# Optimization experiments

Measured on AMD Instinct MI355X. Metric: run time of the kernel, lower is better.

Reference implementation:

```python
import jax, jax.numpy as jnp
import numpy as np

N = 16384       # num_nodes
IN = 128        # in_features
OUT = 128       # out_features
E = 524288      # num edges
NG = 8          # FastKAN num_grids
GRID_MIN, GRID_MAX = -2.0, 2.0
LN_EPS = 1e-5


def setup_inputs() -> dict:
    key = jax.random.key(0)
    ks = jax.random.split(key, 6)
    x = jax.random.normal(ks[0], (N, IN), dtype=jnp.float32)
    edge_index = jax.random.randint(ks[1], (2, E), 0, N, dtype=jnp.int32)
    # FastKANLayer params
    ln_gamma = jnp.ones((IN,), jnp.float32)
    ln_beta = jnp.zeros((IN,), jnp.float32)
    # SplineLinear: trunc-normal-ish init with scale 0.1 (fast-kan default)
    spline_w = (jax.random.normal(ks[2], (OUT, IN * NG), jnp.float32)
                * (0.1 / np.sqrt(IN * NG)))
    base_w = jax.random.normal(ks[3], (OUT, IN), jnp.float32) / np.sqrt(IN)
    base_b = jnp.zeros((OUT,), jnp.float32)
    # GCNConv.bias
    bias = jax.random.normal(ks[4], (OUT,), jnp.float32) * 0.01
    return dict(x=x, edge_index=edge_index, ln_gamma=ln_gamma, ln_beta=ln_beta,
                spline_w=spline_w, base_w=base_w, base_b=base_b, bias=bias)


def _fastkan(x, ln_gamma, ln_beta, spline_w, base_w, base_b):
    # LayerNorm
    mu = jnp.mean(x, axis=-1, keepdims=True)
    var = jnp.mean((x - mu) ** 2, axis=-1, keepdims=True)
    h = (x - mu) * jax.lax.rsqrt(var + LN_EPS) * ln_gamma + ln_beta
    # Gaussian RBF basis over fixed grid
    grid = jnp.linspace(GRID_MIN, GRID_MAX, NG)
    denom = (GRID_MAX - GRID_MIN) / (NG - 1)
    basis = jnp.exp(-(((h[..., None] - grid) / denom) ** 2))  # [N, IN, NG]
    out = basis.reshape(x.shape[0], IN * NG) @ spline_w.T      # [N, OUT]
    out = out + jax.nn.silu(x) @ base_w.T + base_b             # base update
    return out


def reference(x, edge_index, ln_gamma, ln_beta, spline_w, base_w, base_b, bias):
    num_nodes = x.shape[0]
    # Dense symmetric adjacency, exactly as the torch module builds it
    adj = jnp.zeros((num_nodes, num_nodes), x.dtype)
    adj = adj.at[edge_index[0], edge_index[1]].set(1.0)
    adj = adj.at[edge_index[1], edge_index[0]].set(1.0)
    deg = jnp.sum(adj, axis=1)
    dis = 1.0 / jnp.sqrt(deg)
    norm_adj = adj * dis[:, None] * dis[None, :]
    support = _fastkan(x, ln_gamma, ln_beta, spline_w, base_w, base_b)
    return norm_adj @ support + bias
```

## Files before the change

kernel.cpp:

```cpp
#include <hip/hip_runtime.h>

#define N_NODES 16384
#define NE 524288
#define KDIM 1152
#define KPAD 1160
#define KSTEPS 36
#define NBUCK 1024
#define SBLK 512
#define SPB 2048
#define MROW 516
#define DCAP 256

typedef unsigned int uint32;
typedef unsigned short ushort;
typedef __attribute__((ext_vector_type(8))) short bf16x8;
typedef __attribute__((ext_vector_type(4))) float f32x4;

__device__ __forceinline__ ushort f2bf(float f) {
    unsigned u = __float_as_uint(f);
    unsigned r = (u + 0x7fffu + ((u >> 16) & 1u)) >> 16;
    return (ushort)r;
}
__device__ __forceinline__ float bflo(uint32 u) {
    return __uint_as_float(u << 16);
}
__device__ __forceinline__ float bfhi(uint32 u) {
    return __uint_as_float(u & 0xffff0000u);
}

__global__ __launch_bounds__(256) void pre_kernel(
    const int* __restrict__ ei, uint32* __restrict__ ebuf,
    uint32* __restrict__ ocnt, const float* __restrict__ sw,
    const float* __restrict__ bw, ushort* __restrict__ Wp) {
    const int t = threadIdx.x;
    if (blockIdx.x >= SBLK) {
        int idx = (blockIdx.x - SBLK) * 256 + t;
        int i  = idx & 7;
        int l  = (idx >> 3) & 63;
        int ct = (idx >> 9) & 7;
        int kk = idx >> 12;
        int k   = kk * 32 + ((l >> 4) << 3) + i;
        int col = ct * 16 + (l & 15);
        float v = (k < 1024) ? sw[col * 1024 + k] : bw[col * 128 + (k - 1024)];
        Wp[idx] = f2bf(v);
        return;
    }
    __shared__ int hcnt[NBUCK];
    __shared__ int lbase[NBUCK];
    __shared__ int ps[256];
    __shared__ uint32 st[SPB];
    for (int q = t; q < NBUCK; q += 256) hcnt[q] = 0;
    __syncthreads();

    int bk[8], sl[8];
    uint32 pk[8];
#pragma unroll
    for (int k = 0; k < 4; ++k) {
        int e = blockIdx.x * 1024 + k * 256 + t;
        int a = ei[e];
        int b = ei[NE + e];
        bk[2 * k]     = a >> 4;
        pk[2 * k]     = ((uint32)(a & 15) << 14) | (uint32)b;
        bk[2 * k + 1] = b >> 4;
        pk[2 * k + 1] = ((uint32)(b & 15) << 14) | (uint32)a;
        sl[2 * k]     = atomicAdd(&hcnt[bk[2 * k]], 1);
        sl[2 * k + 1] = atomicAdd(&hcnt[bk[2 * k + 1]], 1);
    }
    __syncthreads();

    int c[4], loc[4];
    int s = 0;
#pragma unroll
    for (int q = 0; q < 4; ++q) {
        c[q] = hcnt[t * 4 + q];
        loc[q] = s;
        s += c[q];
    }
    ps[t] = s;
    __syncthreads();
    for (int off = 1; off < 256; off <<= 1) {
        int v = ps[t];
        int add = (t >= off) ? ps[t - off] : 0;
        __syncthreads();
        ps[t] = v + add;
        __syncthreads();
    }
    const int base = (t == 0) ? 0 : ps[t - 1];
    uint32* oc = ocnt + (size_t)blockIdx.x * NBUCK;
#pragma unroll
    for (int q = 0; q < 4; ++q) {
        int e0 = base + loc[q];
        lbase[t * 4 + q] = e0;
        oc[t * 4 + q] = (uint32)e0 | ((uint32)c[q] << 16);
    }
    __syncthreads();

#pragma unroll
    for (int k = 0; k < 8; ++k) st[lbase[bk[k]] + sl[k]] = pk[k];
    __syncthreads();
    uint32* gout = ebuf + (size_t)blockIdx.x * SPB;
#pragma unroll
    for (int k = 0; k < 8; ++k) gout[t + k * 256] = st[t + k * 256];
}

__global__ __launch_bounds__(256) void mid_kernel(
    const uint32* __restrict__ ebuf, const uint32* __restrict__ ocnt,
    float* __restrict__ dis, int* __restrict__ degarr,
    ushort* __restrict__ dadj, const float* __restrict__ x,
    const float* __restrict__ gamma, const float* __restrict__ beta,
    const ushort* __restrict__ Wp, const float* __restrict__ base_b,
    ushort* __restrict__ S) {
    __shared__ __align__(16) ushort smem[16 * KPAD];
    const int t = threadIdx.x;
    const int lane = t & 63;
    const int w = t >> 6;

    if (blockIdx.x & 1) {
        uint32* mask = (uint32*)smem;
        const int bkt = blockIdx.x >> 1;
        for (int i = t; i < 16 * MROW; i += 256) mask[i] = 0;
        __syncthreads();

        for (int b = t; b < SBLK; b += 256) {
            uint32 oc = ocnt[(size_t)b * NBUCK + bkt];
            int off = (int)(oc & 0xFFFFu);
            int cn  = (int)(oc >> 16);
            const uint32* p = ebuf + (size_t)b * SPB + off;
            for (int s = 0; s < cn; ++s) {
                uint32 e = p[s];
                atomicOr(&mask[(e >> 14) * MROW + ((e & 16383) >> 5)],
                         1u << (e & 31));
            }
        }
        __syncthreads();

        for (int n = w * 4; n < w * 4 + 4; ++n) {
            const uint32* row = &mask[n * MROW];
            uint32 wd[8];
            int c = 0;
#pragma unroll
            for (int j = 0; j < 8; ++j) {
                wd[j] = row[lane + 64 * j];
                c += __popc(wd[j]);
            }
            int inc = c;
#pragma unroll
            for (int o = 1; o < 64; o <<= 1) {
                int v = __shfl_up(inc, o);
                if (lane >= o) inc += v;
            }
            int total = __shfl(inc, 63);
            int pos = inc - c;
            const int node = bkt * 16 + n;
            if (lane == 0) {
                dis[node] = rsqrtf((float)total);
                degarr[node] = total > DCAP ? DCAP : total;
            }
            ushort* drow = dadj + (size_t)node * DCAP;
#pragma unroll
            for (int j = 0; j < 8; ++j) {
                uint32 bits = wd[j];
                int base = (lane + 64 * j) * 32;
                while (bits) {
                    int b = __ffs(bits) - 1;
                    bits &= bits - 1;
                    if (pos < DCAP) drow[pos] = (ushort)(base + b);
                    ++pos;
                }
            }
        }
        return;
    }

    ushort* Bs = smem;
    const int nodeBase = (blockIdx.x >> 1) * 16;

    const float g0 = gamma[lane], g1 = gamma[lane + 64];
    const float be0 = beta[lane], be1 = beta[lane + 64];

    for (int n = w * 4; n < w * 4 + 4; ++n) {
        const int row = nodeBase + n;
        float f0 = x[(size_t)row * 128 + lane];
        float f1 = x[(size_t)row * 128 + lane + 64];
        float s = f0 + f1;
#pragma unroll
        for (int o = 32; o; o >>= 1) s += __shfl_xor(s, o);
        float mu = s * 0.0078125f;
        float d0 = f0 - mu, d1 = f1 - mu;
        float v = d0 * d0 + d1 * d1;
#pragma unroll
        for (int o = 32; o; o >>= 1) v += __shfl_xor(v, o);
        float rstd = rsqrtf(v * 0.0078125f + 1e-5f);
        float h0 = d0 * rstd * g0 + be0;
        float h1 = d1 * rstd * g1 + be1;
        ushort pk0[8] __attribute__((aligned(16)));
        ushort pk1[8] __attribute__((aligned(16)));
#pragma unroll
        for (int g = 0; g < 8; ++g) {
            float gv = -2.0f + (float)g * (4.0f / 7.0f);
            float z0 = (h0 - gv) * 1.75f;
            float z1 = (h1 - gv) * 1.75f;
            pk0[g] = f2bf(__expf(-z0 * z0));
            pk1[g] = f2bf(__expf(-z1 * z1));
        }
        *reinterpret_cast<uint4*>(&Bs[n * KPAD + lane * 8]) =
            *reinterpret_cast<const uint4*>(pk0);
        *reinterpret_cast<uint4*>(&Bs[n * KPAD + (lane + 64) * 8]) =
            *reinterpret_cast<const uint4*>(pk1);
        Bs[n * KPAD + 1024 + lane]      = f2bf(f0 / (1.0f + __expf(-f0)));
        Bs[n * KPAD + 1024 + lane + 64] = f2bf(f1 / (1.0f + __expf(-f1)));
    }
    __syncthreads();

    const int ct0 = w * 2;
    f32x4 acc0 = {0.f, 0.f, 0.f, 0.f};
    f32x4 acc1 = {0.f, 0.f, 0.f, 0.f};
    const ushort* ArowBase = &Bs[(lane & 15) * KPAD + (lane >> 4) * 8];
    const bf16x8* Wv = (const bf16x8*)Wp;
#pragma unroll 4
    for (int kk = 0; kk < KSTEPS; ++kk) {
        bf16x8 a = *reinterpret_cast<const bf16x8*>(ArowBase + kk * 32);
        bf16x8 b0 = Wv[(size_t)(kk * 8 + ct0) * 64 + lane];
        bf16x8 b1 = Wv[(size_t)(kk * 8 + ct0 + 1) * 64 + lane];
        acc0 = __builtin_amdgcn_mfma_f32_16x16x32_bf16(a, b0, acc0, 0, 0, 0);
        acc1 = __builtin_amdgcn_mfma_f32_16x16x32_bf16(a, b1, acc1, 0, 0, 0);
    }

    const int col0 = ct0 * 16 + (lane & 15);
    const int rbase = (lane >> 4) * 4;
    const float bb0 = base_b[col0];
    const float bb1 = base_b[col0 + 16];
#pragma unroll
    for (int r = 0; r < 4; ++r) {
        const int row = nodeBase + rbase + r;
        S[(size_t)row * 128 + col0]      = f2bf(acc0[r] + bb0);
        S[(size_t)row * 128 + col0 + 16] = f2bf(acc1[r] + bb1);
    }
}

__global__ __launch_bounds__(256) void aggregate_kernel(
    const int* __restrict__ degarr, const ushort* __restrict__ dadj,
    const ushort* __restrict__ S, const float* __restrict__ dis,
    const float* __restrict__ bias, float* __restrict__ out) {
    __shared__ ushort lst[2][DCAP];
    __shared__ float part[2][2][128];
    const int t = threadIdx.x;
    const int g = t >> 7;
    const int tl = t & 127;
    const int i = blockIdx.x * 2 + g;

    const int total = degarr[i];
    const ushort* drow = dadj + (size_t)i * DCAP;
    if (tl < total) lst[g][tl] = drow[tl];
    if (tl + 128 < total) lst[g][tl + 128] = drow[tl + 128];
    __syncthreads();

    const int lane = t & 63;
    const int wv = (t >> 6) & 1;
    const uint32* S32 = (const uint32*)S;
    float a0 = 0.f, a1 = 0.f;
    int idx = wv;
    for (; idx + 6 < total; idx += 8) {
        int j0 = lst[g][idx], j1 = lst[g][idx + 2];
        int j2 = lst[g][idx + 4], j3 = lst[g][idx + 6];
        float d0 = dis[j0], d1 = dis[j1], d2 = dis[j2], d3 = dis[j3];
        uint32 u0 = S32[(size_t)j0 * 64 + lane];
        uint32 u1 = S32[(size_t)j1 * 64 + lane];
        uint32 u2 = S32[(size_t)j2 * 64 + lane];
        uint32 u3 = S32[(size_t)j3 * 64 + lane];
        a0 += (d0 * bflo(u0) + d1 * bflo(u1)) + (d2 * bflo(u2) + d3 * bflo(u3));
        a1 += (d0 * bfhi(u0) + d1 * bfhi(u1)) + (d2 * bfhi(u2) + d3 * bfhi(u3));
    }
    for (; idx < total; idx += 2) {
        int j = lst[g][idx];
        float d = dis[j];
        uint32 u = S32[(size_t)j * 64 + lane];
        a0 += d * bflo(u);
        a1 += d * bfhi(u);
    }
    part[g][wv][lane * 2]     = a0;
    part[g][wv][lane * 2 + 1] = a1;
    __syncthreads();

    float v = part[g][0][tl] + part[g][1][tl];
    out[(size_t)i * 128 + tl] = v * dis[i] + bias[tl];
}

extern "C" void kernel_launch(void* const* d_in, const int* in_sizes, int n_in,
                              void* d_out, int out_size, void* d_ws, size_t ws_size,
                              hipStream_t stream) {
    const float* x        = (const float*)d_in[0];
    const int*   ei       = (const int*)d_in[1];
    const float* ln_gamma = (const float*)d_in[2];
    const float* ln_beta  = (const float*)d_in[3];
    const float* spline_w = (const float*)d_in[4];
    const float* base_w   = (const float*)d_in[5];
    const float* base_b   = (const float*)d_in[6];
    const float* bias     = (const float*)d_in[7];
    float* out = (float*)d_out;

    char* ws = (char*)d_ws;
    const size_t WP_OFF   = 0;
    const size_t DIS_OFF  = 294912;
    const size_t DEG_OFF  = 360448;
    const size_t DADJ_OFF = 425984;
    const size_t OCNT_OFF = 8814592;
    const size_t EBUF_OFF = 10911744;
    const size_t S_OFF    = 15106048;
    const size_t NEEDED   = 19300352;
    if (ws_size < NEEDED) return;

    ushort* Wp     = (ushort*)(ws + WP_OFF);
    float*  dis    = (float*)(ws + DIS_OFF);
    int*    degarr = (int*)(ws + DEG_OFF);
    ushort* dadj   = (ushort*)(ws + DADJ_OFF);
    uint32* ocnt   = (uint32*)(ws + OCNT_OFF);
    uint32* ebuf   = (uint32*)(ws + EBUF_OFF);
    ushort* S      = (ushort*)(ws + S_OFF);

    pre_kernel<<<SBLK + 576, 256, 0, stream>>>(ei, ebuf, ocnt,
                                               spline_w, base_w, Wp);
    mid_kernel<<<2048, 256, 0, stream>>>(ebuf, ocnt, dis, degarr, dadj,
                                         x, ln_gamma, ln_beta, Wp, base_b, S);
    aggregate_kernel<<<N_NODES / 2, 256, 0, stream>>>(degarr, dadj, S, dis,
                                                      bias, out);
}
```

Baseline: 68.80 us.

## Use fewer, larger edge-bucketing blocks and split mid-kernel bucket scan across threads

Cuts the edge-sorting blocks from 512 to 128, so each block buckets 4096 edges into an 8192-entry shared staging array. Slot assignment now uses a second pass that re-reads the edges and does atomics on the prefix bases, instead of keeping slots in registers. In the mid kernel, each of the 128 source blocks is scanned by two threads with interleaved strides, which shortens the per-bucket serial loop and removes the loop over blocks. The trade-off is reading edge_index twice, using more shared memory per block, and running fewer pre blocks (less parallelism), in exchange for fewer ocnt entries and less serial work in mid_kernel.

```diff
diff --git a/kernel.cpp b/kernel.cpp
--- a/kernel.cpp
+++ b/kernel.cpp
@@ -6,8 +6,8 @@
 #define KPAD 1160
 #define KSTEPS 36
 #define NBUCK 1024
-#define SBLK 512
-#define SPB 2048
+#define SBLK 128
+#define SPB 8192
 #define MROW 516
 #define DCAP 256
 
@@ -46,25 +46,19 @@
         return;
     }
     __shared__ int hcnt[NBUCK];
-    __shared__ int lbase[NBUCK];
     __shared__ int ps[256];
     __shared__ uint32 st[SPB];
     for (int q = t; q < NBUCK; q += 256) hcnt[q] = 0;
     __syncthreads();
 
-    int bk[8], sl[8];
-    uint32 pk[8];
-#pragma unroll
-    for (int k = 0; k < 4; ++k) {
-        int e = blockIdx.x * 1024 + k * 256 + t;
+    const int ebase = blockIdx.x * (NE / SBLK);
+#pragma unroll 4
+    for (int k = 0; k < 16; ++k) {
+        int e = ebase + k * 256 + t;
         int a = ei[e];
         int b = ei[NE + e];
-        bk[2 * k]     = a >> 4;
-        pk[2 * k]     = ((uint32)(a & 15) << 14) | (uint32)b;
-        bk[2 * k + 1] = b >> 4;
-        pk[2 * k + 1] = ((uint32)(b & 15) << 14) | (uint32)a;
-        sl[2 * k]     = atomicAdd(&hcnt[bk[2 * k]], 1);
-        sl[2 * k + 1] = atomicAdd(&hcnt[bk[2 * k + 1]], 1);
+        atomicAdd(&hcnt[a >> 4], 1);
+        atomicAdd(&hcnt[b >> 4], 1);
     }
     __syncthreads();
 
@@ -90,17 +84,26 @@
 #pragma unroll
     for (int q = 0; q < 4; ++q) {
         int e0 = base + loc[q];
-        lbase[t * 4 + q] = e0;
+        hcnt[t * 4 + q] = e0;
         oc[t * 4 + q] = (uint32)e0 | ((uint32)c[q] << 16);
     }
     __syncthreads();
 
-#pragma unroll
-    for (int k = 0; k < 8; ++k) st[lbase[bk[k]] + sl[k]] = pk[k];
-    __syncthreads();
+#pragma unroll 4
+    for (int k = 0; k < 16; ++k) {
+        int e = ebase + k * 256 + t;
+        int a = ei[e];
+        int b = ei[NE + e];
+        int sl = atomicAdd(&hcnt[a >> 4], 1);
+        st[sl] = ((uint32)(a & 15) << 14) | (uint32)b;
+        sl = atomicAdd(&hcnt[b >> 4], 1);
+        st[sl] = ((uint32)(b & 15) << 14) | (uint32)a;
+    }
+    __syncthreads();
+
     uint32* gout = ebuf + (size_t)blockIdx.x * SPB;
 #pragma unroll
-    for (int k = 0; k < 8; ++k) gout[t + k * 256] = st[t + k * 256];
+    for (int k = 0; k < SPB / 256; ++k) gout[t + k * 256] = st[t + k * 256];
 }
 
 __global__ __launch_bounds__(256) void mid_kernel(
@@ -121,12 +124,13 @@
         for (int i = t; i < 16 * MROW; i += 256) mask[i] = 0;
         __syncthreads();
 
-        for (int b = t; b < SBLK; b += 256) {
-            uint32 oc = ocnt[(size_t)b * NBUCK + bkt];
-            int off = (int)(oc & 0xFFFFu);
-            int cn  = (int)(oc >> 16);
+        {
+            const int b = t & 127;
+            const uint32 oc = ocnt[(size_t)b * NBUCK + bkt];
+            const int off = (int)(oc & 0xFFFFu);
+            const int cn  = (int)(oc >> 16);
             const uint32* p = ebuf + (size_t)b * SPB + off;
-            for (int s = 0; s < cn; ++s) {
+            for (int s = (t >> 7); s < cn; s += 2) {
                 uint32 e = p[s];
                 atomicOr(&mask[(e >> 14) * MROW + ((e & 16383) >> 5)],
                          1u << (e & 31));
@@ -305,9 +309,9 @@
     const size_t DEG_OFF  = 360448;
     const size_t DADJ_OFF = 425984;
     const size_t OCNT_OFF = 8814592;
-    const size_t EBUF_OFF = 10911744;
-    const size_t S_OFF    = 15106048;
-    const size_t NEEDED   = 19300352;
+    const size_t EBUF_OFF = 9338880;
+    const size_t S_OFF    = 13533184;
+    const size_t NEEDED   = 17727488;
     if (ws_size < NEEDED) return;
 
     ushort* Wp     = (ushort*)(ws + WP_OFF);
```

After: 74.47 us. 8.2% more time.

## Double GEMM rows per block with split-K LDS phases and 2:1 role mix

Applied to the files above, without the earlier changes.

The GEMM half of mid_kernel now handles 32 nodes per block instead of 16, so each weight fragment loaded from global memory feeds two MFMAs. To keep LDS usage bounded, K is split into two phases of 576, and the weight packing is permuted so each phase covers 64 input channels' RBF and SiLU terms. Block roles change to two adjacency-bucket blocks per GEMM block, which keeps the grid at 1536 blocks. The ocnt loads are also hoisted ahead of the scan loop. The cost is more registers (8 cached rows per wave, 4 accumulators) and an extra barrier between phases.

```diff
diff --git a/kernel.cpp b/kernel.cpp
--- a/kernel.cpp
+++ b/kernel.cpp
@@ -3,8 +3,9 @@
 #define N_NODES 16384
 #define NE 524288
 #define KDIM 1152
-#define KPAD 1160
-#define KSTEPS 36
+#define KPH 576
+#define KPAD2 584
+#define KSTEPS_PH 18
 #define NBUCK 1024
 #define SBLK 512
 #define SPB 2048
@@ -39,9 +40,19 @@
         int l  = (idx >> 3) & 63;
         int ct = (idx >> 9) & 7;
         int kk = idx >> 12;
-        int k   = kk * 32 + ((l >> 4) << 3) + i;
+        int kp  = kk * 32 + ((l >> 4) << 3) + i;
+        int p   = kp / KPH;
+        int r   = kp - p * KPH;
         int col = ct * 16 + (l & 15);
-        float v = (k < 1024) ? sw[col * 1024 + k] : bw[col * 128 + (k - 1024)];
+        float v;
+        if (r < 512) {
+            int ch = p * 64 + (r >> 3);
+            int g  = r & 7;
+            v = sw[col * 1024 + ch * 8 + g];
+        } else {
+            int ch = p * 64 + (r - 512);
+            v = bw[col * 128 + ch];
+        }
         Wp[idx] = f2bf(v);
         return;
     }
@@ -110,19 +121,24 @@
     const float* __restrict__ gamma, const float* __restrict__ beta,
     const ushort* __restrict__ Wp, const float* __restrict__ base_b,
     ushort* __restrict__ S) {
-    __shared__ __align__(16) ushort smem[16 * KPAD];
+    __shared__ __align__(16) ushort smem[32 * KPAD2];
     const int t = threadIdx.x;
     const int lane = t & 63;
     const int w = t >> 6;
-
-    if (blockIdx.x & 1) {
+    const int role = blockIdx.x % 3;
+
+    if (role < 2) {
         uint32* mask = (uint32*)smem;
-        const int bkt = blockIdx.x >> 1;
+        const int bkt = (blockIdx.x / 3) * 2 + role;
         for (int i = t; i < 16 * MROW; i += 256) mask[i] = 0;
         __syncthreads();
 
-        for (int b = t; b < SBLK; b += 256) {
-            uint32 oc = ocnt[(size_t)b * NBUCK + bkt];
+        const uint32 oc0 = ocnt[(size_t)t * NBUCK + bkt];
+        const uint32 oc1 = ocnt[(size_t)(t + 256) * NBUCK + bkt];
+#pragma unroll
+        for (int h = 0; h < 2; ++h) {
+            const int b = h ? (t + 256) : t;
+            const uint32 oc = h ? oc1 : oc0;
             int off = (int)(oc & 0xFFFFu);
             int cn  = (int)(oc >> 16);
             const uint32* p = ebuf + (size_t)b * SPB + off;
@@ -173,13 +189,15 @@
     }
 
     ushort* Bs = smem;
-    const int nodeBase = (blockIdx.x >> 1) * 16;
+    const int nodeBase = (blockIdx.x / 3) * 32;
 
     const float g0 = gamma[lane], g1 = gamma[lane + 64];
     const float be0 = beta[lane], be1 = beta[lane + 64];
 
-    for (int n = w * 4; n < w * 4 + 4; ++n) {
-        const int row = nodeBase + n;
+    float h0r[8], h1r[8], f0r[8], f1r[8];
+#pragma unroll
+    for (int j = 0; j < 8; ++j) {
+        const int row = nodeBase + w * 8 + j;
         float f0 = x[(size_t)row * 128 + lane];
         float f1 = x[(size_t)row * 128 + lane + 64];
         float s = f0 + f1;
@@ -191,39 +209,54 @@
 #pragma unroll
         for (int o = 32; o; o >>= 1) v += __shfl_xor(v, o);
         float rstd = rsqrtf(v * 0.0078125f + 1e-5f);
-        float h0 = d0 * rstd * g0 + be0;
-        float h1 = d1 * rstd * g1 + be1;
-        ushort pk0[8] __attribute__((aligned(16)));
-        ushort pk1[8] __attribute__((aligned(16)));
-#pragma unroll
-        for (int g = 0; g < 8; ++g) {
-            float gv = -2.0f + (float)g * (4.0f / 7.0f);
-            float z0 = (h0 - gv) * 1.75f;
-            float z1 = (h1 - gv) * 1.75f;
-            pk0[g] = f2bf(__expf(-z0 * z0));
-            pk1[g] = f2bf(__expf(-z1 * z1));
-        }
-        *reinterpret_cast<uint4*>(&Bs[n * KPAD + lane * 8]) =
-            *reinterpret_cast<const uint4*>(pk0);
-        *reinterpret_cast<uint4*>(&Bs[n * KPAD + (lane + 64) * 8]) =
-            *reinterpret_cast<const uint4*>(pk1);
-        Bs[n * KPAD + 1024 + lane]      = f2bf(f0 / (1.0f + __expf(-f0)));
-        Bs[n * KPAD + 1024 + lane + 64] = f2bf(f1 / (1.0f + __expf(-f1)));
-    }
-    __syncthreads();
+        h0r[j] = d0 * rstd * g0 + be0;
+        h1r[j] = d1 * rstd * g1 + be1;
+        f0r[j] = f0;
+        f1r[j] = f1;
+    }
 
     const int ct0 = w * 2;
-    f32x4 acc0 = {0.f, 0.f, 0.f, 0.f};
-    f32x4 acc1 = {0.f, 0.f, 0.f, 0.f};
-    const ushort* ArowBase = &Bs[(lane & 15) * KPAD + (lane >> 4) * 8];
+    f32x4 accA = {0.f, 0.f, 0.f, 0.f};
+    f32x4 accB = {0.f, 0.f, 0.f, 0.f};
+    f32x4 accC = {0.f, 0.f, 0.f, 0.f};
+    f32x4 accD = {0.f, 0.f, 0.f, 0.f};
+    const ushort* Alo = &Bs[(lane & 15) * KPAD2 + (lane >> 4) * 8];
+    const ushort* Ahi = Alo + 16 * KPAD2;
     const bf16x8* Wv = (const bf16x8*)Wp;
-#pragma unroll 4
-    for (int kk = 0; kk < KSTEPS; ++kk) {
-        bf16x8 a = *reinterpret_cast<const bf16x8*>(ArowBase + kk * 32);
-        bf16x8 b0 = Wv[(size_t)(kk * 8 + ct0) * 64 + lane];
-        bf16x8 b1 = Wv[(size_t)(kk * 8 + ct0 + 1) * 64 + lane];
-        acc0 = __builtin_amdgcn_mfma_f32_16x16x32_bf16(a, b0, acc0, 0, 0, 0);
-        acc1 = __builtin_amdgcn_mfma_f32_16x16x32_bf16(a, b1, acc1, 0, 0, 0);
+
+#pragma unroll
+    for (int p = 0; p < 2; ++p) {
+        if (p) __syncthreads();
+#pragma unroll
+        for (int j = 0; j < 8; ++j) {
+            const int n = w * 8 + j;
+            const float h = p ? h1r[j] : h0r[j];
+            const float f = p ? f1r[j] : f0r[j];
+            ushort pk[8] __attribute__((aligned(16)));
+#pragma unroll
+            for (int g = 0; g < 8; ++g) {
+                float gv = -2.0f + (float)g * (4.0f / 7.0f);
+                float z = (h - gv) * 1.75f;
+                pk[g] = f2bf(__expf(-z * z));
+            }
+            *reinterpret_cast<uint4*>(&Bs[n * KPAD2 + lane * 8]) =
+                *reinterpret_cast<const uint4*>(pk);
+            Bs[n * KPAD2 + 512 + lane] = f2bf(f / (1.0f + __expf(-f)));
+        }
+        __syncthreads();
+
+#pragma unroll 3
+        for (int kkl = 0; kkl < KSTEPS_PH; ++kkl) {
+            const int kkg = p * KSTEPS_PH + kkl;
+            bf16x8 alo = *reinterpret_cast<const bf16x8*>(Alo + kkl * 32);
+            bf16x8 ahi = *reinterpret_cast<const bf16x8*>(Ahi + kkl * 32);
+            bf16x8 b0 = Wv[(size_t)(kkg * 8 + ct0) * 64 + lane];
+            bf16x8 b1 = Wv[(size_t)(kkg * 8 + ct0 + 1) * 64 + lane];
+            accA = __builtin_amdgcn_mfma_f32_16x16x32_bf16(alo, b0, accA, 0, 0, 0);
+            accB = __builtin_amdgcn_mfma_f32_16x16x32_bf16(alo, b1, accB, 0, 0, 0);
+            accC = __builtin_amdgcn_mfma_f32_16x16x32_bf16(ahi, b0, accC, 0, 0, 0);
+            accD = __builtin_amdgcn_mfma_f32_16x16x32_bf16(ahi, b1, accD, 0, 0, 0);
+        }
     }
 
     const int col0 = ct0 * 16 + (lane & 15);
@@ -232,9 +265,12 @@
     const float bb1 = base_b[col0 + 16];
 #pragma unroll
     for (int r = 0; r < 4; ++r) {
-        const int row = nodeBase + rbase + r;
-        S[(size_t)row * 128 + col0]      = f2bf(acc0[r] + bb0);
-        S[(size_t)row * 128 + col0 + 16] = f2bf(acc1[r] + bb1);
+        const int rlo = nodeBase + rbase + r;
+        const int rhi = rlo + 16;
+        S[(size_t)rlo * 128 + col0]      = f2bf(accA[r] + bb0);
+        S[(size_t)rlo * 128 + col0 + 16] = f2bf(accB[r] + bb1);
+        S[(size_t)rhi * 128 + col0]      = f2bf(accC[r] + bb0);
+        S[(size_t)rhi * 128 + col0 + 16] = f2bf(accD[r] + bb1);
     }
 }
 
@@ -320,7 +356,7 @@
 
     pre_kernel<<<SBLK + 576, 256, 0, stream>>>(ei, ebuf, ocnt,
                                                spline_w, base_w, Wp);
-    mid_kernel<<<2048, 256, 0, stream>>>(ebuf, ocnt, dis, degarr, dadj,
+    mid_kernel<<<1536, 256, 0, stream>>>(ebuf, ocnt, dis, degarr, dadj,
                                          x, ln_gamma, ln_beta, Wp, base_b, S);
     aggregate_kernel<<<N_NODES / 2, 256, 0, stream>>>(degarr, dadj, S, dis,
                                                       bias, out);
```

Result: faster. 66.88 us (-2.8%).
